# Kernel tuning notes

Measured on AMD Instinct MI355X. Metric: run time of the kernel, lower is better.

The kernel has to match this reference:

```python
import jax, jax.numpy as jnp
import numpy as np
from jax import lax

B, INC1, INC2, H, W = 8, 64, 128, 128, 128
EPS = 1e-5  # BatchNorm eps; inference mode with running_mean=0, running_var=1


def leaky(x):
    return jnp.where(x >= 0, x, 0.01 * x)


def conv2d(x, w, pad=0, dil=1, groups=1):
    return lax.conv_general_dilated(
        x, w, (1, 1), [(pad, pad), (pad, pad)], rhs_dilation=(dil, dil),
        dimension_numbers=('NCHW', 'OIHW', 'NCHW'), feature_group_count=groups)


def bnlrelu(x, g, b):
    s = g / jnp.sqrt(1.0 + EPS)
    return leaky(x * s[None, :, None, None] + b[None, :, None, None])


def interp_bilinear_ac(x, oh, ow):
    # bilinear, align_corners=True (matches F.interpolate)
    ih, iw = x.shape[-2], x.shape[-1]
    ys = jnp.linspace(0.0, ih - 1.0, oh)
    xs = jnp.linspace(0.0, iw - 1.0, ow)
    y0 = jnp.floor(ys).astype(jnp.int32); y1 = jnp.minimum(y0 + 1, ih - 1)
    x0 = jnp.floor(xs).astype(jnp.int32); x1 = jnp.minimum(x0 + 1, iw - 1)
    wy = (ys - y0)[:, None]; wx = xs - x0
    rows = x[..., y0, :] * (1.0 - wy) + x[..., y1, :] * wy
    return rows[..., x0] * (1.0 - wx) + rows[..., x1] * wx


def se_layer(x, w1, w2):
    y = x.mean(axis=(2, 3))                     # [B, C]
    y = jax.nn.sigmoid(leaky(y @ w1.T) @ w2.T)  # squeeze-excite gates
    return x * y[:, :, None, None]


def dyn_multidil(f2, k):
    # per-sample depthwise conv with input-dependent 5x5 kernels, 3 dilations
    C = k.shape[1]
    def per_sample(fi, ki):
        xi = fi[None]            # [1, C, H, W]
        wi = ki[:, None, :, :]   # [C, 1, 5, 5]
        r = conv2d(xi, wi, pad=2, dil=1, groups=C)
        r = r + conv2d(xi, wi, pad=4, dil=2, groups=C)
        r = r + conv2d(xi, wi, pad=6, dil=3, groups=C)
        return r[0]
    out = jax.vmap(per_sample)(f2, k)
    return out.at[0].set(f2[0])  # original python loop starts at i=1: sample 0 untouched


def _forward(x1, k, conv1_w, conv1_g, conv1_b, conv2_w, conv2_g, conv2_b,
             conv_w, conv_bias, c0_w, c0_g, c0_b, attc_w, attc_g, attc_b,
             c05_w, c05_g, c05_b, conv0a_w, conv0a_g, conv0a_b,
             conv0b_w, conv0b_g, conv0b_b, se_w1, se_w2):
    h, w = x1.shape[2], x1.shape[3]
    kse = interp_bilinear_ac(k, h, w)                       # [B, inc1, H, W]
    va = x1.mean(axis=(2, 3), keepdims=True)                # AdaptiveAvgPool2d(1)
    bias = conv_bias[None, :, None, None]
    # MaxPool2d(1) is identity, so conv(vm) == conv(x1); bias added in both terms
    fuseadd = (conv2d(va, conv_w) + bias) + (conv2d(x1, conv_w) + bias)
    fuseadd = fuseadd * kse + fuseadd
    att = jax.nn.sigmoid(fuseadd)
    eadd = bnlrelu(conv2d(fuseadd, c0_w, pad=1), c0_g, c0_b)
    A1 = jax.nn.sigmoid(bnlrelu(conv2d(eadd, attc_w, pad=1), attc_g, attc_b))
    att = se_layer(att, se_w1, se_w2)
    f1 = bnlrelu(conv2d(x1, conv1_w), conv1_g, conv1_b)
    f2 = bnlrelu(conv2d(x1, conv2_w), conv2_g, conv2_b)
    out1 = bnlrelu(conv2d(f1, c0_w, pad=1), c0_g, c0_b)
    out1 = out1 * kse + out1
    A2 = jax.nn.sigmoid(bnlrelu(conv2d(out1, attc_w, pad=1), attc_g, attc_b))
    out2 = dyn_multidil(f2, k)
    out2 = out2 * kse + out2
    out2conv = bnlrelu(conv2d(out2, c05_w, pad=2), c05_g, c05_b)
    fuseout2 = A1 * A2 * out2conv
    finout2 = bnlrelu(conv2d(fuseout2, c05_w, pad=2), c05_g, c05_b)
    eout2 = finout2 + out2conv + f2
    out2 = bnlrelu(conv2d(eout2, c05_w, pad=2), c05_g, c05_b)
    out = jnp.concatenate([out1, out2], axis=1)             # [B, 2*inc1, H, W]
    out = bnlrelu(conv2d(out, conv0a_w), conv0a_g, conv0a_b)
    out = bnlrelu(conv2d(out, conv0b_w, pad=1), conv0b_g, conv0b_b)
    return att * out * A1


def setup_inputs() -> dict:
    key = jax.random.key(0)
    ks = jax.random.split(key, 32)
    f32 = jnp.float32
    def w(i, shape, s=0.05):
        return jax.random.normal(ks[i], shape, f32) * s
    return {
        'x1': jax.random.normal(ks[0], (B, INC2, H, W), f32),
        'k': jax.random.normal(ks[1], (B, INC1, 5, 5), f32) * 0.2,
        'conv1_w': w(2, (INC1, INC2, 1, 1)),
        'conv1_g': 1.0 + w(3, (INC1,)),
        'conv1_b': w(4, (INC1,)),
        'conv2_w': w(5, (INC1, INC2, 1, 1)),
        'conv2_g': 1.0 + w(6, (INC1,)),
        'conv2_b': w(7, (INC1,)),
        'conv_w': w(8, (INC1, INC2, 1, 1)),
        'conv_bias': w(9, (INC1,)),
        'c0_w': w(10, (INC1, INC1, 3, 3)),
        'c0_g': 1.0 + w(11, (INC1,)),
        'c0_b': w(12, (INC1,)),
        'attc_w': w(13, (INC1, INC1, 3, 3)),
        'attc_g': 1.0 + w(14, (INC1,)),
        'attc_b': w(15, (INC1,)),
        'c05_w': w(16, (INC1, INC1, 5, 5)),
        'c05_g': 1.0 + w(17, (INC1,)),
        'c05_b': w(18, (INC1,)),
        'conv0a_w': w(19, (INC1, 2 * INC1, 1, 1)),
        'conv0a_g': 1.0 + w(20, (INC1,)),
        'conv0a_b': w(21, (INC1,)),
        'conv0b_w': w(22, (INC1, INC1, 3, 3)),
        'conv0b_g': 1.0 + w(23, (INC1,)),
        'conv0b_b': w(24, (INC1,)),
        'se_w1': w(25, (INC1 // 16, INC1)),
        'se_w2': w(26, (INC1, INC1 // 16)),
    }


def reference(x1, k, conv1_w, conv1_g, conv1_b, conv2_w, conv2_g, conv2_b,
              conv_w, conv_bias, c0_w, c0_g, c0_b, attc_w, attc_g, attc_b,
              c05_w, c05_g, c05_b, conv0a_w, conv0a_g, conv0a_b,
              conv0b_w, conv0b_g, conv0b_b, se_w1, se_w2):
    return _forward(x1, k, conv1_w, conv1_g, conv1_b, conv2_w, conv2_g, conv2_b,
                    conv_w, conv_bias, c0_w, c0_g, c0_b, attc_w, attc_g, attc_b,
                    c05_w, c05_g, c05_b, conv0a_w, conv0a_g, conv0a_b,
                    conv0b_w, conv0b_g, conv0b_b, se_w1, se_w2)
```

## Files before the change

### kernel.cpp

```cpp
#include <hip/hip_runtime.h>
#include <math.h>

#define HW 16384
#define EPSC 1.00001f

typedef short bf16x8 __attribute__((ext_vector_type(8)));
typedef float f32x4 __attribute__((ext_vector_type(4)));

static __device__ __forceinline__ unsigned short f2bf(float f) {
    unsigned int u = __float_as_uint(f);
    unsigned int r = (u + 0x7fffu + ((u >> 16) & 1u)) >> 16;
    return (unsigned short)r;
}
static __device__ __forceinline__ float bf2f(unsigned short u) {
    return __uint_as_float(((unsigned int)u) << 16);
}

__global__ void mean_hw_kernel(const float* __restrict__ x, float* __restrict__ out) {
    int blk = blockIdx.x;
    const float4* p4 = (const float4*)(x + (size_t)blk * HW);
    float s = 0.f;
    for (int i = threadIdx.x; i < HW / 4; i += 256) {
        float4 v = p4[i];
        s += v.x + v.y + v.z + v.w;
    }
    for (int off = 32; off > 0; off >>= 1) s += __shfl_down(s, off, 64);
    __shared__ float red[4];
    int lane = threadIdx.x & 63, wid = threadIdx.x >> 6;
    if (lane == 0) red[wid] = s;
    __syncthreads();
    if (threadIdx.x == 0)
        out[blk] = (red[0] + red[1] + red[2] + red[3]) * (1.0f / (float)HW);
}

__global__ void convva_kernel(const float* __restrict__ va, const float* __restrict__ cw,
                              float* __restrict__ out) {
    int t = threadIdx.x;
    int b = t >> 6, co = t & 63;
    float s = 0.f;
    for (int ci = 0; ci < 128; ci++) s = fmaf(cw[co * 128 + ci], va[b * 128 + ci], s);
    out[t] = s;
}

__global__ void att_mean_part(const unsigned short* __restrict__ att0, float* __restrict__ part) {
    int s = blockIdx.x, b = blockIdx.y;
    int c = threadIdx.x & 63, pr = threadIdx.x >> 6;
    const unsigned short* p = att0 + ((size_t)b * HW + s * 1024 + pr * 256) * 64 + c;
    float acc = 0.f;
    for (int i = 0; i < 256; i++) acc += bf2f(p[(size_t)i * 64]);
    __shared__ float red[4][64];
    red[pr][c] = acc;
    __syncthreads();
    if (threadIdx.x < 64)
        part[(b * 16 + s) * 64 + threadIdx.x] =
            red[0][threadIdx.x] + red[1][threadIdx.x] + red[2][threadIdx.x] + red[3][threadIdx.x];
}

__global__ void se_mlp_kernel(const float* __restrict__ part, const float* __restrict__ w1,
                              const float* __restrict__ w2, float* __restrict__ scale) {
    __shared__ float t[8][4];
    __shared__ float ym[8][64];
    int tid = threadIdx.x;
    {
        int b = tid >> 6, c = tid & 63;
        float s = 0.f;
        for (int i = 0; i < 16; i++) s += part[(b * 16 + i) * 64 + c];
        ym[b][c] = s * (1.0f / (float)HW);
    }
    __syncthreads();
    if (tid < 32) {
        int b = tid >> 2, h = tid & 3;
        float s = 0.f;
        for (int ci = 0; ci < 64; ci++) s = fmaf(ym[b][ci], w1[h * 64 + ci], s);
        t[b][h] = s >= 0.f ? s : 0.01f * s;
    }
    __syncthreads();
    int b = tid >> 6, c = tid & 63;
    float s = 0.f;
    for (int h = 0; h < 4; h++) s = fmaf(t[b][h], w2[c * 4 + h], s);
    scale[b * 64 + c] = 1.0f / (1.0f + __expf(-s));
}

__device__ __forceinline__ float kse_val(const float* kt, int y, int x) {
    float ys = y * (4.0f / 127.0f);
    int y0 = (int)ys; if (y0 > 4) y0 = 4;
    int y1 = min(y0 + 1, 4);
    float wy = ys - (float)y0;
    float xs = x * (4.0f / 127.0f);
    int x0 = (int)xs; if (x0 > 4) x0 = 4;
    int x1 = min(x0 + 1, 4);
    float wx = xs - (float)x0;
    float r0 = kt[y0 * 5 + x0] * (1.f - wx) + kt[y0 * 5 + x1] * wx;
    float r1 = kt[y1 * 5 + x0] * (1.f - wx) + kt[y1 * 5 + x1] * wx;
    return r0 * (1.f - wy) + r1 * wy;
}

__global__ void repack_x1_kernel(const float* __restrict__ x1,
                                 unsigned short* __restrict__ xa,
                                 unsigned short* __restrict__ xb) {
    __shared__ float t[64][65];
    int b = blockIdx.y;
    int p0 = blockIdx.x * 64;
    for (int h = 0; h < 2; ++h) {
        const float* src = x1 + ((size_t)b * 128 + h * 64) * HW + p0;
        __syncthreads();
        for (int e = threadIdx.x; e < 4096; e += 256) {
            int ci = e >> 6, px = e & 63;
            t[ci][px] = src[(size_t)ci * HW + px];
        }
        __syncthreads();
        unsigned short* dst = (h == 0 ? xa : xb) + ((size_t)b * HW + p0) * 64;
        for (int e = threadIdx.x; e < 4096; e += 256) {
            int px = e >> 6, ci = e & 63;
            dst[(size_t)px * 64 + ci] = f2bf(t[ci][px]);
        }
    }
}

__global__ void prep_w_kernel(const float* __restrict__ src, unsigned short* __restrict__ dst,
                              int CO, int CI, int K, int co_total, int co_off) {
    int idx = blockIdx.x * 256 + threadIdx.x;
    int total = CO * CI * K * K;
    if (idx >= total) return;
    int kx = idx % K, t1 = idx / K;
    int ky = t1 % K, t2 = t1 / K;
    int ci = t2 % CI, co = t2 / CI;
    int tap = ky * K + kx, chunk = ci >> 5, k32 = ci & 31;
    int kc = tap * (CI >> 5) + chunk;
    dst[((size_t)kc * co_total + co_off + co) * 32 + k32] = f2bf(src[idx]);
}

template<int KSZ, int CI>
__global__ __launch_bounds__(256, 3) void conv_mfma(
    const unsigned short* __restrict__ Xa, const unsigned short* __restrict__ Xb,
    const unsigned short* __restrict__ Wp,
    const float* __restrict__ g, const float* __restrict__ bb,
    const float* __restrict__ kk,
    const unsigned short* __restrict__ eB, const unsigned short* __restrict__ eC,
    float* __restrict__ out_f32, unsigned short* __restrict__ out_bf,
    unsigned short* __restrict__ aux_bf, int emode)
{
    constexpr int TH  = 8;
    constexpr int PAD = KSZ / 2;
    constexpr int TWX = 16 + 2 * PAD;
    constexpr int TWY = TH + 2 * PAD;
    constexpr int CHUNKS = CI / 32;
    constexpr int NT = 2;
    constexpr int CI8 = CI / 8;
    constexpr int CI8SH = (CI == 64) ? 3 : 4;
    constexpr int NTAP = KSZ * KSZ;
    constexpr int WSLAB = 64 * 32 * CHUNKS;
    constexpr int NBUF = (KSZ == 1) ? 1 : 2;
    constexpr int NSTG = WSLAB / (8 * 256);
    __shared__ unsigned short xs[TWY * TWX * CI];
    __shared__ unsigned short ws[NBUF * WSLAB];

    const int b = blockIdx.y;
    const int ty = (blockIdx.x >> 3) * TH, tx = (blockIdx.x & 7) * 16;
    const int tid = threadIdx.x;
    const int lane = tid & 63, wv = tid >> 6;
    const int n = lane & 15, quad = lane >> 4;

    uint4 wst[NSTG];
    {
        const uint4* gw = (const uint4*)Wp;
#pragma unroll
        for (int s = 0; s < NSTG; ++s) wst[s] = gw[tid + s * 256];
    }
    for (int e = tid; e < TWY * TWX * CI8; e += 256) {
        int ci8 = e & (CI8 - 1);
        int pxl = e >> CI8SH;
        int xx = pxl % TWX, yy = pxl / TWX;
        int gy = ty + yy - PAD, gx = tx + xx - PAD;
        uint4 v = {0u, 0u, 0u, 0u};
        if (gy >= 0 && gy < 128 && gx >= 0 && gx < 128) {
            const unsigned short* src = Xa;
            int c8 = ci8;
            if (CI == 128 && ci8 >= 8) { src = Xb; c8 = ci8 - 8; }
            v = *(const uint4*)(src + (((size_t)b * HW + gy * 128 + gx) * 64 + c8 * 8));
        }
        *(uint4*)(&xs[(size_t)pxl * CI + ((ci8 ^ (pxl & 7)) << 3)]) = v;
    }
    {
        uint4* lw = (uint4*)ws;
#pragma unroll
        for (int s = 0; s < NSTG; ++s) lw[tid + s * 256] = wst[s];
    }
    __syncthreads();

    f32x4 acc[4][NT];
#pragma unroll
    for (int mb = 0; mb < 4; ++mb)
#pragma unroll
        for (int nt = 0; nt < NT; ++nt) acc[mb][nt] = (f32x4){0.f, 0.f, 0.f, 0.f};

    const int r0 = wv * NT;
    for (int tap = 0; tap < NTAP; ++tap) {
        if (KSZ > 1 && tap + 1 < NTAP) {
            const uint4* gw = (const uint4*)Wp + (size_t)(tap + 1) * (WSLAB / 8);
#pragma unroll
            for (int s = 0; s < NSTG; ++s) wst[s] = gw[tid + s * 256];
        }
        const unsigned short* wl = ws + ((NBUF == 2) ? (tap & 1) * WSLAB : 0);
        const int ky = tap / KSZ, kx = tap - ky * KSZ;
#pragma unroll
        for (int ch = 0; ch < CHUNKS; ++ch) {
            bf16x8 af[4];
#pragma unroll
            for (int mb = 0; mb < 4; ++mb)
                af[mb] = *(const bf16x8*)(wl + (ch * 64 + mb * 16 + n) * 32 + quad * 8);
            bf16x8 bfr[NT];
#pragma unroll
            for (int nt = 0; nt < NT; ++nt) {
                int pxl = (r0 + nt + ky) * TWX + n + kx;
                bfr[nt] = *(const bf16x8*)(&xs[(size_t)pxl * CI +
                                               (((ch * 4 + quad) ^ (pxl & 7)) << 3)]);
            }
#pragma unroll
            for (int mb = 0; mb < 4; ++mb)
#pragma unroll
                for (int nt = 0; nt < NT; ++nt)
                    acc[mb][nt] = __builtin_amdgcn_mfma_f32_16x16x32_bf16(
                        af[mb], bfr[nt], acc[mb][nt], 0, 0, 0);
        }
        if (KSZ > 1 && tap + 1 < NTAP) {
            uint4* lw = (uint4*)(ws + ((tap + 1) & 1) * WSLAB);
#pragma unroll
            for (int s = 0; s < NSTG; ++s) lw[tid + s * 256] = wst[s];
            __syncthreads();
        }
    }

    const float rs = rsqrtf(EPSC);
#pragma unroll
    for (int mb = 0; mb < 4; ++mb) {
#pragma unroll
        for (int nt = 0; nt < NT; ++nt) {
            const int py = ty + r0 + nt;
            const int px = tx + n;
            const size_t pix = (size_t)b * HW + py * 128 + px;
            const int co0 = mb * 16 + quad * 4;
            float v4[4];
#pragma unroll
            for (int rg = 0; rg < 4; ++rg) {
                int co = co0 + rg;
                float v = acc[mb][nt][rg];
                v = fmaf(v, g[co] * rs, bb[co]);
                v = v >= 0.f ? v : 0.01f * v;
                if (emode == 1 || emode == 6) v = 1.0f / (1.0f + __expf(-v));
                else if (emode == 2)
                    v *= (1.0f + kse_val(kk + (size_t)(b * 64 + co) * 25, py, px));
                v4[rg] = v;
            }
            if (emode == 6) {
                ushort4 e = *(const ushort4*)(eB + pix * 64 + co0);
                *(ushort4*)(out_bf + pix * 64 + co0) = (ushort4){
                    f2bf(v4[0] * bf2f(e.x)), f2bf(v4[1] * bf2f(e.y)),
                    f2bf(v4[2] * bf2f(e.z)), f2bf(v4[3] * bf2f(e.w))};
            } else if (emode == 4) {
                *(ushort4*)(out_bf + pix * 64 + co0) =
                    (ushort4){f2bf(v4[0]), f2bf(v4[1]), f2bf(v4[2]), f2bf(v4[3])};
                ushort4 e = *(const ushort4*)(eB + pix * 64 + co0);
                *(ushort4*)(aux_bf + pix * 64 + co0) = (ushort4){
                    f2bf(v4[0] * bf2f(e.x)), f2bf(v4[1] * bf2f(e.y)),
                    f2bf(v4[2] * bf2f(e.z)), f2bf(v4[3] * bf2f(e.w))};
            } else if (emode == 5) {
                ushort4 e1 = *(const ushort4*)(eB + pix * 64 + co0);
                ushort4 e2 = *(const ushort4*)(eC + pix * 64 + co0);
                *(ushort4*)(out_bf + pix * 64 + co0) = (ushort4){
                    f2bf(v4[0] + bf2f(e1.x) + bf2f(e2.x)), f2bf(v4[1] + bf2f(e1.y) + bf2f(e2.y)),
                    f2bf(v4[2] + bf2f(e1.z) + bf2f(e2.z)), f2bf(v4[3] + bf2f(e1.w) + bf2f(e2.w))};
            } else {
                if (out_bf)
                    *(ushort4*)(out_bf + pix * 64 + co0) =
                        (ushort4){f2bf(v4[0]), f2bf(v4[1]), f2bf(v4[2]), f2bf(v4[3])};
                if (out_f32) {
#pragma unroll
                    for (int rg = 0; rg < 4; ++rg)
                        out_f32[(size_t)(b * 64 + co0 + rg) * HW + py * 128 + px] = v4[rg];
                }
            }
        }
    }
}

__global__ __launch_bounds__(256, 2) void conv1x1_triple(
    const unsigned short* __restrict__ Xa, const unsigned short* __restrict__ Xb,
    const unsigned short* __restrict__ Wp,
    const float* __restrict__ cva, const float* __restrict__ cbias,
    const float* __restrict__ g1, const float* __restrict__ b1,
    const float* __restrict__ g2, const float* __restrict__ b2,
    const float* __restrict__ kk,
    unsigned short* __restrict__ fuse_bf, unsigned short* __restrict__ att0_bf,
    unsigned short* __restrict__ f1_bf,
    float* __restrict__ f2_f32, unsigned short* __restrict__ f2_bf)
{
    constexpr int CI = 128;
    __shared__ unsigned short xs[128 * CI];
    __shared__ unsigned short ws[4 * 192 * 32];
    const int b = blockIdx.y;
    const int ty = (blockIdx.x >> 3) * 8, tx = (blockIdx.x & 7) * 16;
    const int tid = threadIdx.x;
    const int lane = tid & 63, wv = tid >> 6;
    const int n = lane & 15, quad = lane >> 4;

    {
        const uint4* gw = (const uint4*)Wp;
        uint4* lw = (uint4*)ws;
#pragma unroll
        for (int s = 0; s < 12; ++s) lw[tid + s * 256] = gw[tid + s * 256];
    }
    for (int e = tid; e < 128 * 16; e += 256) {
        int ci8 = e & 15, pxl = e >> 4;
        int gy = ty + (pxl >> 4), gx = tx + (pxl & 15);
        const unsigned short* src = (ci8 >= 8) ? Xb : Xa;
        int c8 = ci8 & 7;
        uint4 v = *(const uint4*)(src + (((size_t)b * HW + gy * 128 + gx) * 64 + c8 * 8));
        *(uint4*)(&xs[(size_t)pxl * CI + ((ci8 ^ (pxl & 7)) << 3)]) = v;
    }
    __syncthreads();

    f32x4 acc[12][2];
#pragma unroll
    for (int mb = 0; mb < 12; ++mb)
#pragma unroll
        for (int nt = 0; nt < 2; ++nt) acc[mb][nt] = (f32x4){0.f, 0.f, 0.f, 0.f};

    const int r0 = wv * 2;
#pragma unroll
    for (int ch = 0; ch < 4; ++ch) {
        bf16x8 bfr[2];
#pragma unroll
        for (int nt = 0; nt < 2; ++nt) {
            int pxl = (r0 + nt) * 16 + n;
            bfr[nt] = *(const bf16x8*)(&xs[(size_t)pxl * CI +
                                           (((ch * 4 + quad) ^ (pxl & 7)) << 3)]);
        }
#pragma unroll
        for (int mb = 0; mb < 12; ++mb) {
            bf16x8 af = *(const bf16x8*)(ws + (ch * 192 + mb * 16 + n) * 32 + quad * 8);
#pragma unroll
            for (int nt = 0; nt < 2; ++nt)
                acc[mb][nt] = __builtin_amdgcn_mfma_f32_16x16x32_bf16(
                    af, bfr[nt], acc[mb][nt], 0, 0, 0);
        }
    }

    const float rs = rsqrtf(EPSC);
#pragma unroll
    for (int mb = 0; mb < 12; ++mb) {
#pragma unroll
        for (int nt = 0; nt < 2; ++nt) {
            const int py = ty + r0 + nt;
            const int px = tx + n;
            const size_t pix = (size_t)b * HW + py * 128 + px;
            const int cg = mb * 16 + quad * 4;
            if (mb < 4) {
                float v4[4], s4[4];
#pragma unroll
                for (int rg = 0; rg < 4; ++rg) {
                    int co = cg + rg;
                    float base = cva[b * 64 + co] + 2.0f * cbias[co];
                    float fa = (acc[mb][nt][rg] + base) *
                               (1.0f + kse_val(kk + (size_t)(b * 64 + co) * 25, py, px));
                    v4[rg] = fa;
                    s4[rg] = 1.0f / (1.0f + __expf(-fa));
                }
                *(ushort4*)(fuse_bf + pix * 64 + cg) =
                    (ushort4){f2bf(v4[0]), f2bf(v4[1]), f2bf(v4[2]), f2bf(v4[3])};
                *(ushort4*)(att0_bf + pix * 64 + cg) =
                    (ushort4){f2bf(s4[0]), f2bf(s4[1]), f2bf(s4[2]), f2bf(s4[3])};
            } else if (mb < 8) {
                int co0 = cg - 64;
                float v4[4];
#pragma unroll
                for (int rg = 0; rg < 4; ++rg) {
                    float v = fmaf(acc[mb][nt][rg], g1[co0 + rg] * rs, b1[co0 + rg]);
                    v4[rg] = v >= 0.f ? v : 0.01f * v;
                }
                *(ushort4*)(f1_bf + pix * 64 + co0) =
                    (ushort4){f2bf(v4[0]), f2bf(v4[1]), f2bf(v4[2]), f2bf(v4[3])};
            } else {
                int co0 = cg - 128;
                float v4[4];
#pragma unroll
                for (int rg = 0; rg < 4; ++rg) {
                    float v = fmaf(acc[mb][nt][rg], g2[co0 + rg] * rs, b2[co0 + rg]);
                    v4[rg] = v >= 0.f ? v : 0.01f * v;
                    f2_f32[(size_t)(b * 64 + co0 + rg) * HW + py * 128 + px] = v4[rg];
                }
                *(ushort4*)(f2_bf + pix * 64 + co0) =
                    (ushort4){f2bf(v4[0]), f2bf(v4[1]), f2bf(v4[2]), f2bf(v4[3])};
            }
        }
    }
}

__global__ __launch_bounds__(256) void dyndil_kernel(const float* __restrict__ f2,
                                                     const float* __restrict__ kk,
                                                     unsigned short* __restrict__ out2bf) {
    __shared__ float xl[44][148];
    int b = blockIdx.x >> 8, c = (blockIdx.x >> 2) & 63, band = blockIdx.x & 3;
    int y0 = band * 32;
    int tid = threadIdx.x;
    int r = tid >> 3, s = tid & 7;
    int x0 = s * 16;
    int y = y0 + r;
    const float* xp = f2 + (size_t)(b * 64 + c) * HW;
    const float* kt = kk + (size_t)(b * 64 + c) * 25;
    float acc[16];

    if (b != 0) {
        for (int e = tid; e < 44 * 148; e += 256) {
            int rr = e / 148, cc = e - rr * 148;
            int yy = y0 + rr - 6, xx = cc - 8;
            float v = 0.f;
            if (yy >= 0 && yy < 128 && xx >= 0 && xx < 128)
                v = xp[yy * 128 + xx];
            xl[rr][cc] = v;
        }
        float kw[25];
#pragma unroll
        for (int i = 0; i < 25; i++) kw[i] = kt[i];
        __syncthreads();
#pragma unroll
        for (int e = 0; e < 16; e++) acc[e] = 0.f;
        int rr = r + 6;
        float win[32];
#define LOADROW(OFF) { const float4* p4 = (const float4*)&xl[rr + (OFF)][x0]; \
        float4 t0=p4[0],t1=p4[1],t2=p4[2],t3=p4[3],t4=p4[4],t5=p4[5],t6=p4[6],t7=p4[7]; \
        win[0]=t0.x;win[1]=t0.y;win[2]=t0.z;win[3]=t0.w; win[4]=t1.x;win[5]=t1.y;win[6]=t1.z;win[7]=t1.w; \
        win[8]=t2.x;win[9]=t2.y;win[10]=t2.z;win[11]=t2.w; win[12]=t3.x;win[13]=t3.y;win[14]=t3.z;win[15]=t3.w; \
        win[16]=t4.x;win[17]=t4.y;win[18]=t4.z;win[19]=t4.w; win[20]=t5.x;win[21]=t5.y;win[22]=t5.z;win[23]=t5.w; \
        win[24]=t6.x;win[25]=t6.y;win[26]=t6.z;win[27]=t6.w; win[28]=t7.x;win[29]=t7.y;win[30]=t7.z;win[31]=t7.w; }
#define APPLY(DIL, I) { \
        _Pragma("unroll") for (int j = 0; j < 5; j++) { \
            float wv = kw[(I)*5 + j]; int o = 8 + (j - 2) * (DIL); \
            _Pragma("unroll") for (int e2 = 0; e2 < 16; e2++) \
                acc[e2] = fmaf(wv, win[e2 + o], acc[e2]); } }
        LOADROW(-6) APPLY(3,0)
        LOADROW(-4) APPLY(2,0)
        LOADROW(-3) APPLY(3,1)
        LOADROW(-2) APPLY(1,0) APPLY(2,1)
        LOADROW(-1) APPLY(1,1)
        LOADROW(0)  APPLY(1,2) APPLY(2,2) APPLY(3,2)
        LOADROW(1)  APPLY(1,3)
        LOADROW(2)  APPLY(1,4) APPLY(2,3)
        LOADROW(3)  APPLY(3,3)
        LOADROW(4)  APPLY(2,4)
        LOADROW(6)  APPLY(3,4)
#undef LOADROW
#undef APPLY
    } else {
        const float4* p4 = (const float4*)(xp + y * 128 + x0);
#pragma unroll
        for (int i = 0; i < 4; i++) {
            float4 v = p4[i];
            acc[i*4] = v.x; acc[i*4+1] = v.y; acc[i*4+2] = v.z; acc[i*4+3] = v.w;
        }
    }
    float ys = y * (4.0f / 127.0f);
    int yi0 = (int)ys; if (yi0 > 4) yi0 = 4;
    int yi1 = yi0 + 1; if (yi1 > 4) yi1 = 4;
    float wy = ys - (float)yi0;
    float ry0 = kt[yi0*5+0] * (1.f-wy) + kt[yi1*5+0] * wy;
    float ry1 = kt[yi0*5+1] * (1.f-wy) + kt[yi1*5+1] * wy;
    float ry2 = kt[yi0*5+2] * (1.f-wy) + kt[yi1*5+2] * wy;
    float ry3 = kt[yi0*5+3] * (1.f-wy) + kt[yi1*5+3] * wy;
    float ry4 = kt[yi0*5+4] * (1.f-wy) + kt[yi1*5+4] * wy;
    unsigned short* op = out2bf + ((size_t)b * HW + (size_t)y * 128 + x0) * 64 + c;
#pragma unroll
    for (int e = 0; e < 16; e++) {
        int x = x0 + e;
        float xs2 = x * (4.0f / 127.0f);
        int xi0 = (int)xs2; if (xi0 > 4) xi0 = 4;
        float wx = xs2 - (float)xi0;
        float a = xi0==0 ? ry0 : xi0==1 ? ry1 : xi0==2 ? ry2 : xi0==3 ? ry3 : ry4;
        float bs = xi0>=3 ? ry4 : (xi0==2 ? ry3 : (xi0==1 ? ry2 : ry1));
        float kv = a + (bs - a) * wx;
        op[(size_t)e * 64] = f2bf(acc[e] * (1.0f + kv));
    }
}

__global__ void final_kernel(const unsigned short* __restrict__ att0,
                             const float* __restrict__ scale,
                             const unsigned short* __restrict__ outb,
                             const unsigned short* __restrict__ a1,
                             float* __restrict__ o) {
    __shared__ float t[64][65];
    int b = blockIdx.y;
    int p0 = blockIdx.x * 64;
    int tid = threadIdx.x;
    for (int e = tid; e < 4096; e += 256) {
        int px = e >> 6, c = e & 63;
        size_t idx = ((size_t)b * HW + p0 + px) * 64 + c;
        t[c][px] = bf2f(att0[idx]) * scale[b * 64 + c] * bf2f(outb[idx]) * bf2f(a1[idx]);
    }
    __syncthreads();
    for (int e = tid; e < 4096; e += 256) {
        int c = e >> 6, px = e & 63;
        o[((size_t)b * 64 + c) * HW + p0 + px] = t[c][px];
    }
}

extern "C" void kernel_launch(void* const* d_in, const int* in_sizes, int n_in,
                              void* d_out, int out_size, void* d_ws, size_t ws_size,
                              hipStream_t stream) {
    const float* x1      = (const float*)d_in[0];
    const float* kk      = (const float*)d_in[1];
    const float* conv1_w = (const float*)d_in[2];
    const float* conv1_g = (const float*)d_in[3];
    const float* conv1_b = (const float*)d_in[4];
    const float* conv2_w = (const float*)d_in[5];
    const float* conv2_g = (const float*)d_in[6];
    const float* conv2_b = (const float*)d_in[7];
    const float* conv_w  = (const float*)d_in[8];
    const float* conv_bias = (const float*)d_in[9];
    const float* c0_w  = (const float*)d_in[10];
    const float* c0_g  = (const float*)d_in[11];
    const float* c0_b  = (const float*)d_in[12];
    const float* attc_w = (const float*)d_in[13];
    const float* attc_g = (const float*)d_in[14];
    const float* attc_b = (const float*)d_in[15];
    const float* c05_w = (const float*)d_in[16];
    const float* c05_g = (const float*)d_in[17];
    const float* c05_b = (const float*)d_in[18];
    const float* conv0a_w = (const float*)d_in[19];
    const float* conv0a_g = (const float*)d_in[20];
    const float* conv0a_b = (const float*)d_in[21];
    const float* conv0b_w = (const float*)d_in[22];
    const float* conv0b_g = (const float*)d_in[23];
    const float* conv0b_b = (const float*)d_in[24];
    const float* se_w1 = (const float*)d_in[25];
    const float* se_w2 = (const float*)d_in[26];

    const size_t U = (size_t)8 * HW * 64 * 2;
    unsigned char* P = (unsigned char*)d_ws;
    unsigned short* x1a        = (unsigned short*)(P + 0 * U);
    unsigned short* x1b        = (unsigned short*)(P + 1 * U);
    unsigned short* att0_bf    = (unsigned short*)(P + 2 * U);
    unsigned short* fuse_bf    = (unsigned short*)(P + 3 * U);
    unsigned short* f1_bf      = (unsigned short*)(P + 4 * U);
    float*          f2         = (float*)         (P + 5 * U);
    unsigned short* f2_bf      = (unsigned short*)(P + 7 * U);
    unsigned short* A1_bf      = (unsigned short*)(P + 8 * U);
    unsigned short* eadd_bf    = (unsigned short*)(P + 9 * U);
    unsigned short* out1_bf    = (unsigned short*)(P + 10 * U);
    unsigned short* A12_bf     = (unsigned short*)(P + 11 * U);
    unsigned short* out2_bf     = x1a;
    unsigned short* oc_bf       = x1b;
    unsigned short* fuseout2_bf = fuse_bf;
    unsigned short* eout2_bf    = f1_bf;
    unsigned short* out2fin_bf  = eadd_bf;
    unsigned short* outb_bf     = out1_bf;
    unsigned short* outa_bf     = A12_bf;

    unsigned char* W0 = P + 12 * U;
    unsigned short* Wp1   = (unsigned short*)(W0);
    unsigned short* Wc0   = (unsigned short*)(W0 + 49152);
    unsigned short* Wattc = (unsigned short*)(W0 + 122880);
    unsigned short* Wc05  = (unsigned short*)(W0 + 196608);
    unsigned short* Wc0a  = (unsigned short*)(W0 + 401408);
    unsigned short* Wc0b  = (unsigned short*)(W0 + 417792);
    float* va   = (float*)(W0 + 491520);
    float* cva  = va + 1024;
    float* part = cva + 512;
    float* sesc = part + 8192;

    const dim3 gconv(128, 8);

    mean_hw_kernel<<<1024, 256, 0, stream>>>(x1, va);
    convva_kernel<<<1, 512, 0, stream>>>(va, conv_w, cva);
    repack_x1_kernel<<<dim3(256, 8), 256, 0, stream>>>(x1, x1a, x1b);
    prep_w_kernel<<<32, 256, 0, stream>>>(conv_w,   Wp1, 64, 128, 1, 192, 0);
    prep_w_kernel<<<32, 256, 0, stream>>>(conv1_w,  Wp1, 64, 128, 1, 192, 64);
    prep_w_kernel<<<32, 256, 0, stream>>>(conv2_w,  Wp1, 64, 128, 1, 192, 128);
    prep_w_kernel<<<144, 256, 0, stream>>>(c0_w,    Wc0,   64, 64, 3, 64, 0);
    prep_w_kernel<<<144, 256, 0, stream>>>(attc_w,  Wattc, 64, 64, 3, 64, 0);
    prep_w_kernel<<<400, 256, 0, stream>>>(c05_w,   Wc05,  64, 64, 5, 64, 0);
    prep_w_kernel<<<32, 256, 0, stream>>>(conv0a_w, Wc0a,  64, 128, 1, 64, 0);
    prep_w_kernel<<<144, 256, 0, stream>>>(conv0b_w, Wc0b, 64, 64, 3, 64, 0);

    conv1x1_triple<<<gconv, 256, 0, stream>>>(x1a, x1b, Wp1, cva, conv_bias,
        conv1_g, conv1_b, conv2_g, conv2_b, kk, fuse_bf, att0_bf, f1_bf, f2, f2_bf);

    att_mean_part<<<dim3(16, 8), 256, 0, stream>>>(att0_bf, part);
    se_mlp_kernel<<<1, 512, 0, stream>>>(part, se_w1, se_w2, sesc);

    dyndil_kernel<<<2048, 256, 0, stream>>>(f2, kk, out2_bf);

    conv_mfma<3, 64><<<gconv, 256, 0, stream>>>(fuse_bf, nullptr, Wc0,
        c0_g, c0_b, kk, nullptr, nullptr, nullptr, eadd_bf, nullptr, 0);
    conv_mfma<3, 64><<<gconv, 256, 0, stream>>>(eadd_bf, nullptr, Wattc,
        attc_g, attc_b, kk, nullptr, nullptr, nullptr, A1_bf, nullptr, 1);
    conv_mfma<3, 64><<<gconv, 256, 0, stream>>>(f1_bf, nullptr, Wc0,
        c0_g, c0_b, kk, nullptr, nullptr, nullptr, out1_bf, nullptr, 2);
    conv_mfma<3, 64><<<gconv, 256, 0, stream>>>(out1_bf, nullptr, Wattc,
        attc_g, attc_b, kk, A1_bf, nullptr, nullptr, A12_bf, nullptr, 6);

    conv_mfma<5, 64><<<gconv, 256, 0, stream>>>(out2_bf, nullptr, Wc05,
        c05_g, c05_b, kk, A12_bf, nullptr, nullptr, oc_bf, fuseout2_bf, 4);
    conv_mfma<5, 64><<<gconv, 256, 0, stream>>>(fuseout2_bf, nullptr, Wc05,
        c05_g, c05_b, kk, oc_bf, f2_bf, nullptr, eout2_bf, nullptr, 5);
    conv_mfma<5, 64><<<gconv, 256, 0, stream>>>(eout2_bf, nullptr, Wc05,
        c05_g, c05_b, kk, nullptr, nullptr, nullptr, out2fin_bf, nullptr, 0);

    conv_mfma<1, 128><<<gconv, 256, 0, stream>>>(out1_bf, out2fin_bf, Wc0a,
        conv0a_g, conv0a_b, kk, nullptr, nullptr, nullptr, outa_bf, nullptr, 0);
    conv_mfma<3, 64><<<gconv, 256, 0, stream>>>(outa_bf, nullptr, Wc0b,
        conv0b_g, conv0b_b, kk, nullptr, nullptr, nullptr, outb_bf, nullptr, 0);
    final_kernel<<<dim3(256, 8), 256, 0, stream>>>(att0_bf, sesc, outb_bf, A1_bf, (float*)d_out);
}
```

Before: 633.7 us.

## Switch spatial convs to 32x32x16 MFMA with 16x16 tiles and lane-packed weights

The 3x3 and 5x5 convolutions move from 16x16x32 MFMA on 8x16 pixel tiles to 32x32x16 MFMA on 16x16 tiles. Each wave now computes 64 pixels by 64 output channels. Weights are repacked per lane so A fragments load with contiguous, conflict-free LDS reads, and the halo overhead per output pixel drops. The 1x1 conv gets its own specialised kernel with preloaded lane-packed weights. The cost is more accumulator registers, occupancy lowered to 2 blocks per SM, and half as many blocks (512) spread over the GPU.

```diff
diff --git a/kernel.cpp b/kernel.cpp
--- a/kernel.cpp
+++ b/kernel.cpp
@@ -6,6 +6,7 @@
 
 typedef short bf16x8 __attribute__((ext_vector_type(8)));
 typedef float f32x4 __attribute__((ext_vector_type(4)));
+typedef float f32x16 __attribute__((ext_vector_type(16)));
 
 static __device__ __forceinline__ unsigned short f2bf(float f) {
     unsigned int u = __float_as_uint(f);
@@ -130,104 +131,227 @@
     dst[((size_t)kc * co_total + co_off + co) * 32 + k32] = f2bf(src[idx]);
 }
 
-template<int KSZ, int CI>
-__global__ __launch_bounds__(256, 3) void conv_mfma(
-    const unsigned short* __restrict__ Xa, const unsigned short* __restrict__ Xb,
+__global__ void prep_w32_kernel(const float* __restrict__ src, unsigned short* __restrict__ dst,
+                                int CO, int CI, int K) {
+    int idx = blockIdx.x * 256 + threadIdx.x;
+    int total = CO * CI * K * K;
+    if (idx >= total) return;
+    int kx = idx % K, t1 = idx / K;
+    int ky = t1 % K, t2 = t1 / K;
+    int ci = t2 % CI, co = t2 / CI;
+    int tap = ky * K + kx;
+    int kstep = ci >> 4, khalf = (ci >> 3) & 1, j = ci & 7;
+    int l = khalf * 32 + (co & 31), mb = co >> 5;
+    dst[(((size_t)(tap * 4 + kstep) * 2 + mb) * 64 + l) * 8 + j] = f2bf(src[idx]);
+}
+
+__global__ void prep_w16_kernel(const float* __restrict__ src, unsigned short* __restrict__ dst,
+                                int CO, int CI) {
+    int idx = blockIdx.x * 256 + threadIdx.x;
+    if (idx >= CO * CI) return;
+    int ci = idx % CI, co = idx / CI;
+    int ch = ci >> 5, q = (ci >> 3) & 3, j = ci & 7;
+    int l = q * 16 + (co & 15), mb = co >> 4;
+    dst[(((size_t)ch * 4 + mb) * 64 + l) * 8 + j] = f2bf(src[idx]);
+}
+
+template<int KSZ>
+__global__ __launch_bounds__(256, 2) void conv_mfma32(
+    const unsigned short* __restrict__ Xa,
     const unsigned short* __restrict__ Wp,
     const float* __restrict__ g, const float* __restrict__ bb,
     const float* __restrict__ kk,
     const unsigned short* __restrict__ eB, const unsigned short* __restrict__ eC,
-    float* __restrict__ out_f32, unsigned short* __restrict__ out_bf,
-    unsigned short* __restrict__ aux_bf, int emode)
+    unsigned short* __restrict__ out_bf, unsigned short* __restrict__ aux_bf, int emode)
 {
-    constexpr int TH  = 8;
     constexpr int PAD = KSZ / 2;
     constexpr int TWX = 16 + 2 * PAD;
-    constexpr int TWY = TH + 2 * PAD;
-    constexpr int CHUNKS = CI / 32;
-    constexpr int NT = 2;
-    constexpr int CI8 = CI / 8;
-    constexpr int CI8SH = (CI == 64) ? 3 : 4;
+    constexpr int TWY = 16 + 2 * PAD;
     constexpr int NTAP = KSZ * KSZ;
-    constexpr int WSLAB = 64 * 32 * CHUNKS;
-    constexpr int NBUF = (KSZ == 1) ? 1 : 2;
-    constexpr int NSTG = WSLAB / (8 * 256);
-    __shared__ unsigned short xs[TWY * TWX * CI];
-    __shared__ unsigned short ws[NBUF * WSLAB];
+    constexpr int WSLAB = 4 * 2 * 64 * 8;
+    __shared__ unsigned short xs[TWY * TWX * 64];
+    __shared__ unsigned short ws[2 * WSLAB];
 
     const int b = blockIdx.y;
-    const int ty = (blockIdx.x >> 3) * TH, tx = (blockIdx.x & 7) * 16;
+    const int ty = (blockIdx.x >> 3) * 16, tx = (blockIdx.x & 7) * 16;
+    const int tid = threadIdx.x;
+    const int lane = tid & 63, wv = tid >> 6;
+    const int n32 = lane & 31, khalf = lane >> 5;
+
+    int rr[2], cc2[2];
+#pragma unroll
+    for (int nt = 0; nt < 2; ++nt) {
+        int p = wv * 64 + nt * 32 + n32;
+        rr[nt] = p >> 4; cc2[nt] = p & 15;
+    }
+
+    uint4 wst[2];
+    {
+        const uint4* gw = (const uint4*)Wp;
+#pragma unroll
+        for (int s = 0; s < 2; ++s) wst[s] = gw[tid + s * 256];
+    }
+    for (int e = tid; e < TWY * TWX * 8; e += 256) {
+        int ci8 = e & 7, pxl = e >> 3;
+        int xx = pxl % TWX, yy = pxl / TWX;
+        int gy = ty + yy - PAD, gx = tx + xx - PAD;
+        uint4 v = {0u, 0u, 0u, 0u};
+        if (gy >= 0 && gy < 128 && gx >= 0 && gx < 128)
+            v = *(const uint4*)(Xa + (((size_t)b * HW + gy * 128 + gx) * 64 + ci8 * 8));
+        *(uint4*)(&xs[(size_t)pxl * 64 + ((ci8 ^ (pxl & 7)) << 3)]) = v;
+    }
+    {
+        uint4* lw = (uint4*)ws;
+#pragma unroll
+        for (int s = 0; s < 2; ++s) lw[tid + s * 256] = wst[s];
+    }
+    __syncthreads();
+
+    f32x16 acc[2][2];
+#pragma unroll
+    for (int mb = 0; mb < 2; ++mb)
+#pragma unroll
+        for (int nt = 0; nt < 2; ++nt)
+#pragma unroll
+            for (int i = 0; i < 16; ++i) acc[mb][nt][i] = 0.f;
+
+    for (int tap = 0; tap < NTAP; ++tap) {
+        if (tap + 1 < NTAP) {
+            const uint4* gw = (const uint4*)Wp + (size_t)(tap + 1) * (WSLAB / 8);
+#pragma unroll
+            for (int s = 0; s < 2; ++s) wst[s] = gw[tid + s * 256];
+        }
+        const unsigned short* wl = ws + (tap & 1) * WSLAB;
+        const int ky = tap / KSZ, kx = tap - ky * KSZ;
+        int pxl0 = (rr[0] + ky) * TWX + cc2[0] + kx;
+        int pxl1 = (rr[1] + ky) * TWX + cc2[1] + kx;
+        int sw0 = (pxl0 & 7), sw1 = (pxl1 & 7);
+#pragma unroll
+        for (int kstep = 0; kstep < 4; ++kstep) {
+            bf16x8 af0 = *(const bf16x8*)(wl + ((kstep * 2 + 0) * 64 + lane) * 8);
+            bf16x8 af1 = *(const bf16x8*)(wl + ((kstep * 2 + 1) * 64 + lane) * 8);
+            int gidx = kstep * 2 + khalf;
+            bf16x8 b0 = *(const bf16x8*)(&xs[(size_t)pxl0 * 64 + ((gidx ^ sw0) << 3)]);
+            bf16x8 b1 = *(const bf16x8*)(&xs[(size_t)pxl1 * 64 + ((gidx ^ sw1) << 3)]);
+            acc[0][0] = __builtin_amdgcn_mfma_f32_32x32x16_bf16(af0, b0, acc[0][0], 0, 0, 0);
+            acc[0][1] = __builtin_amdgcn_mfma_f32_32x32x16_bf16(af0, b1, acc[0][1], 0, 0, 0);
+            acc[1][0] = __builtin_amdgcn_mfma_f32_32x32x16_bf16(af1, b0, acc[1][0], 0, 0, 0);
+            acc[1][1] = __builtin_amdgcn_mfma_f32_32x32x16_bf16(af1, b1, acc[1][1], 0, 0, 0);
+        }
+        if (tap + 1 < NTAP) {
+            uint4* lw = (uint4*)(ws + ((tap + 1) & 1) * WSLAB);
+#pragma unroll
+            for (int s = 0; s < 2; ++s) lw[tid + s * 256] = wst[s];
+            __syncthreads();
+        }
+    }
+
+    const float rs = rsqrtf(EPSC);
+#pragma unroll
+    for (int mb = 0; mb < 2; ++mb) {
+#pragma unroll
+        for (int nt = 0; nt < 2; ++nt) {
+            const int py = ty + rr[nt];
+            const int px = tx + cc2[nt];
+            const size_t pix = (size_t)b * HW + py * 128 + px;
+#pragma unroll
+            for (int rq = 0; rq < 4; ++rq) {
+                const int co0 = mb * 32 + rq * 8 + khalf * 4;
+                float v4[4];
+#pragma unroll
+                for (int rg = 0; rg < 4; ++rg) {
+                    int co = co0 + rg;
+                    float v = acc[mb][nt][rq * 4 + rg];
+                    v = fmaf(v, g[co] * rs, bb[co]);
+                    v = v >= 0.f ? v : 0.01f * v;
+                    if (emode == 1 || emode == 6) v = 1.0f / (1.0f + __expf(-v));
+                    else if (emode == 2)
+                        v *= (1.0f + kse_val(kk + (size_t)(b * 64 + co) * 25, py, px));
+                    v4[rg] = v;
+                }
+                if (emode == 6) {
+                    ushort4 e = *(const ushort4*)(eB + pix * 64 + co0);
+                    *(ushort4*)(out_bf + pix * 64 + co0) = (ushort4){
+                        f2bf(v4[0] * bf2f(e.x)), f2bf(v4[1] * bf2f(e.y)),
+                        f2bf(v4[2] * bf2f(e.z)), f2bf(v4[3] * bf2f(e.w))};
+                } else if (emode == 4) {
+                    *(ushort4*)(out_bf + pix * 64 + co0) =
+                        (ushort4){f2bf(v4[0]), f2bf(v4[1]), f2bf(v4[2]), f2bf(v4[3])};
+                    ushort4 e = *(const ushort4*)(eB + pix * 64 + co0);
+                    *(ushort4*)(aux_bf + pix * 64 + co0) = (ushort4){
+                        f2bf(v4[0] * bf2f(e.x)), f2bf(v4[1] * bf2f(e.y)),
+                        f2bf(v4[2] * bf2f(e.z)), f2bf(v4[3] * bf2f(e.w))};
+                } else if (emode == 5) {
+                    ushort4 e1 = *(const ushort4*)(eB + pix * 64 + co0);
+                    ushort4 e2 = *(const ushort4*)(eC + pix * 64 + co0);
+                    *(ushort4*)(out_bf + pix * 64 + co0) = (ushort4){
+                        f2bf(v4[0] + bf2f(e1.x) + bf2f(e2.x)),
+                        f2bf(v4[1] + bf2f(e1.y) + bf2f(e2.y)),
+                        f2bf(v4[2] + bf2f(e1.z) + bf2f(e2.z)),
+                        f2bf(v4[3] + bf2f(e1.w) + bf2f(e2.w))};
+                } else {
+                    *(ushort4*)(out_bf + pix * 64 + co0) =
+                        (ushort4){f2bf(v4[0]), f2bf(v4[1]), f2bf(v4[2]), f2bf(v4[3])};
+                }
+            }
+        }
+    }
+}
+
+__global__ __launch_bounds__(256, 2) void conv_mfma1x1(
+    const unsigned short* __restrict__ Xa, const unsigned short* __restrict__ Xb,
+    const unsigned short* __restrict__ Wp,
+    const float* __restrict__ g, const float* __restrict__ bb,
+    unsigned short* __restrict__ out_bf)
+{
+    constexpr int CI = 128;
+    __shared__ unsigned short xs[128 * CI];
+    __shared__ unsigned short ws[4 * 4 * 64 * 8];
+    const int b = blockIdx.y;
+    const int ty = (blockIdx.x >> 3) * 8, tx = (blockIdx.x & 7) * 16;
     const int tid = threadIdx.x;
     const int lane = tid & 63, wv = tid >> 6;
     const int n = lane & 15, quad = lane >> 4;
 
-    uint4 wst[NSTG];
     {
         const uint4* gw = (const uint4*)Wp;
-#pragma unroll
-        for (int s = 0; s < NSTG; ++s) wst[s] = gw[tid + s * 256];
-    }
-    for (int e = tid; e < TWY * TWX * CI8; e += 256) {
-        int ci8 = e & (CI8 - 1);
-        int pxl = e >> CI8SH;
-        int xx = pxl % TWX, yy = pxl / TWX;
-        int gy = ty + yy - PAD, gx = tx + xx - PAD;
-        uint4 v = {0u, 0u, 0u, 0u};
-        if (gy >= 0 && gy < 128 && gx >= 0 && gx < 128) {
-            const unsigned short* src = Xa;
-            int c8 = ci8;
-            if (CI == 128 && ci8 >= 8) { src = Xb; c8 = ci8 - 8; }
-            v = *(const uint4*)(src + (((size_t)b * HW + gy * 128 + gx) * 64 + c8 * 8));
-        }
+        uint4* lw = (uint4*)ws;
+#pragma unroll
+        for (int s = 0; s < 4; ++s) lw[tid + s * 256] = gw[tid + s * 256];
+    }
+    for (int e = tid; e < 128 * 16; e += 256) {
+        int ci8 = e & 15, pxl = e >> 4;
+        int gy = ty + (pxl >> 4), gx = tx + (pxl & 15);
+        const unsigned short* src = (ci8 >= 8) ? Xb : Xa;
+        int c8 = ci8 & 7;
+        uint4 v = *(const uint4*)(src + (((size_t)b * HW + gy * 128 + gx) * 64 + c8 * 8));
         *(uint4*)(&xs[(size_t)pxl * CI + ((ci8 ^ (pxl & 7)) << 3)]) = v;
     }
-    {
-        uint4* lw = (uint4*)ws;
-#pragma unroll
-        for (int s = 0; s < NSTG; ++s) lw[tid + s * 256] = wst[s];
-    }
     __syncthreads();
 
-    f32x4 acc[4][NT];
+    f32x4 acc[4][2];
 #pragma unroll
     for (int mb = 0; mb < 4; ++mb)
 #pragma unroll
-        for (int nt = 0; nt < NT; ++nt) acc[mb][nt] = (f32x4){0.f, 0.f, 0.f, 0.f};
-
-    const int r0 = wv * NT;
-    for (int tap = 0; tap < NTAP; ++tap) {
-        if (KSZ > 1 && tap + 1 < NTAP) {
-            const uint4* gw = (const uint4*)Wp + (size_t)(tap + 1) * (WSLAB / 8);
-#pragma unroll
-            for (int s = 0; s < NSTG; ++s) wst[s] = gw[tid + s * 256];
-        }
-        const unsigned short* wl = ws + ((NBUF == 2) ? (tap & 1) * WSLAB : 0);
-        const int ky = tap / KSZ, kx = tap - ky * KSZ;
-#pragma unroll
-        for (int ch = 0; ch < CHUNKS; ++ch) {
-            bf16x8 af[4];
-#pragma unroll
-            for (int mb = 0; mb < 4; ++mb)
-                af[mb] = *(const bf16x8*)(wl + (ch * 64 + mb * 16 + n) * 32 + quad * 8);
-            bf16x8 bfr[NT];
-#pragma unroll
-            for (int nt = 0; nt < NT; ++nt) {
-                int pxl = (r0 + nt + ky) * TWX + n + kx;
-                bfr[nt] = *(const bf16x8*)(&xs[(size_t)pxl * CI +
-                                               (((ch * 4 + quad) ^ (pxl & 7)) << 3)]);
-            }
-#pragma unroll
-            for (int mb = 0; mb < 4; ++mb)
-#pragma unroll
-                for (int nt = 0; nt < NT; ++nt)
-                    acc[mb][nt] = __builtin_amdgcn_mfma_f32_16x16x32_bf16(
-                        af[mb], bfr[nt], acc[mb][nt], 0, 0, 0);
-        }
-        if (KSZ > 1 && tap + 1 < NTAP) {
-            uint4* lw = (uint4*)(ws + ((tap + 1) & 1) * WSLAB);
-#pragma unroll
-            for (int s = 0; s < NSTG; ++s) lw[tid + s * 256] = wst[s];
-            __syncthreads();
+        for (int nt = 0; nt < 2; ++nt) acc[mb][nt] = (f32x4){0.f, 0.f, 0.f, 0.f};
+
+    const int r0 = wv * 2;
+#pragma unroll
+    for (int ch = 0; ch < 4; ++ch) {
+        bf16x8 bfr[2];
+#pragma unroll
+        for (int nt = 0; nt < 2; ++nt) {
+            int pxl = (r0 + nt) * 16 + n;
+            bfr[nt] = *(const bf16x8*)(&xs[(size_t)pxl * CI +
+                                           (((ch * 4 + quad) ^ (pxl & 7)) << 3)]);
+        }
+#pragma unroll
+        for (int mb = 0; mb < 4; ++mb) {
+            bf16x8 af = *(const bf16x8*)(ws + ((ch * 4 + mb) * 64 + lane) * 8);
+#pragma unroll
+            for (int nt = 0; nt < 2; ++nt)
+                acc[mb][nt] = __builtin_amdgcn_mfma_f32_16x16x32_bf16(
+                    af, bfr[nt], acc[mb][nt], 0, 0, 0);
         }
     }
 
@@ -235,51 +359,18 @@
 #pragma unroll
     for (int mb = 0; mb < 4; ++mb) {
 #pragma unroll
-        for (int nt = 0; nt < NT; ++nt) {
-            const int py = ty + r0 + nt;
-            const int px = tx + n;
+        for (int nt = 0; nt < 2; ++nt) {
+            const int py = ty + r0 + nt, px = tx + n;
             const size_t pix = (size_t)b * HW + py * 128 + px;
             const int co0 = mb * 16 + quad * 4;
             float v4[4];
 #pragma unroll
             for (int rg = 0; rg < 4; ++rg) {
-                int co = co0 + rg;
-                float v = acc[mb][nt][rg];
-                v = fmaf(v, g[co] * rs, bb[co]);
-                v = v >= 0.f ? v : 0.01f * v;
-                if (emode == 1 || emode == 6) v = 1.0f / (1.0f + __expf(-v));
-                else if (emode == 2)
-                    v *= (1.0f + kse_val(kk + (size_t)(b * 64 + co) * 25, py, px));
-                v4[rg] = v;
+                float v = fmaf(acc[mb][nt][rg], g[co0 + rg] * rs, bb[co0 + rg]);
+                v4[rg] = v >= 0.f ? v : 0.01f * v;
             }
-            if (emode == 6) {
-                ushort4 e = *(const ushort4*)(eB + pix * 64 + co0);
-                *(ushort4*)(out_bf + pix * 64 + co0) = (ushort4){
-                    f2bf(v4[0] * bf2f(e.x)), f2bf(v4[1] * bf2f(e.y)),
-                    f2bf(v4[2] * bf2f(e.z)), f2bf(v4[3] * bf2f(e.w))};
-            } else if (emode == 4) {
-                *(ushort4*)(out_bf + pix * 64 + co0) =
-                    (ushort4){f2bf(v4[0]), f2bf(v4[1]), f2bf(v4[2]), f2bf(v4[3])};
-                ushort4 e = *(const ushort4*)(eB + pix * 64 + co0);
-                *(ushort4*)(aux_bf + pix * 64 + co0) = (ushort4){
-                    f2bf(v4[0] * bf2f(e.x)), f2bf(v4[1] * bf2f(e.y)),
-                    f2bf(v4[2] * bf2f(e.z)), f2bf(v4[3] * bf2f(e.w))};
-            } else if (emode == 5) {
-                ushort4 e1 = *(const ushort4*)(eB + pix * 64 + co0);
-                ushort4 e2 = *(const ushort4*)(eC + pix * 64 + co0);
-                *(ushort4*)(out_bf + pix * 64 + co0) = (ushort4){
-                    f2bf(v4[0] + bf2f(e1.x) + bf2f(e2.x)), f2bf(v4[1] + bf2f(e1.y) + bf2f(e2.y)),
-                    f2bf(v4[2] + bf2f(e1.z) + bf2f(e2.z)), f2bf(v4[3] + bf2f(e1.w) + bf2f(e2.w))};
-            } else {
-                if (out_bf)
-                    *(ushort4*)(out_bf + pix * 64 + co0) =
-                        (ushort4){f2bf(v4[0]), f2bf(v4[1]), f2bf(v4[2]), f2bf(v4[3])};
-                if (out_f32) {
-#pragma unroll
-                    for (int rg = 0; rg < 4; ++rg)
-                        out_f32[(size_t)(b * 64 + co0 + rg) * HW + py * 128 + px] = v4[rg];
-                }
-            }
+            *(ushort4*)(out_bf + pix * 64 + co0) =
+                (ushort4){f2bf(v4[0]), f2bf(v4[1]), f2bf(v4[2]), f2bf(v4[3])};
         }
     }
 }
@@ -567,7 +658,8 @@
     float* part = cva + 512;
     float* sesc = part + 8192;
 
-    const dim3 gconv(128, 8);
+    const dim3 g32(64, 8);
+    const dim3 g16(128, 8);
 
     mean_hw_kernel<<<1024, 256, 0, stream>>>(x1, va);
     convva_kernel<<<1, 512, 0, stream>>>(va, conv_w, cva);
@@ -575,13 +667,13 @@
     prep_w_kernel<<<32, 256, 0, stream>>>(conv_w,   Wp1, 64, 128, 1, 192, 0);
     prep_w_kernel<<<32, 256, 0, stream>>>(conv1_w,  Wp1, 64, 128, 1, 192, 64);
     prep_w_kernel<<<32, 256, 0, stream>>>(conv2_w,  Wp1, 64, 128, 1, 192, 128);
-    prep_w_kernel<<<144, 256, 0, stream>>>(c0_w,    Wc0,   64, 64, 3, 64, 0);
-    prep_w_kernel<<<144, 256, 0, stream>>>(attc_w,  Wattc, 64, 64, 3, 64, 0);
-    prep_w_kernel<<<400, 256, 0, stream>>>(c05_w,   Wc05,  64, 64, 5, 64, 0);
-    prep_w_kernel<<<32, 256, 0, stream>>>(conv0a_w, Wc0a,  64, 128, 1, 64, 0);
-    prep_w_kernel<<<144, 256, 0, stream>>>(conv0b_w, Wc0b, 64, 64, 3, 64, 0);
-
-    conv1x1_triple<<<gconv, 256, 0, stream>>>(x1a, x1b, Wp1, cva, conv_bias,
+    prep_w32_kernel<<<144, 256, 0, stream>>>(c0_w,    Wc0,   64, 64, 3);
+    prep_w32_kernel<<<144, 256, 0, stream>>>(attc_w,  Wattc, 64, 64, 3);
+    prep_w32_kernel<<<400, 256, 0, stream>>>(c05_w,   Wc05,  64, 64, 5);
+    prep_w16_kernel<<<32, 256, 0, stream>>>(conv0a_w, Wc0a,  64, 128);
+    prep_w32_kernel<<<144, 256, 0, stream>>>(conv0b_w, Wc0b, 64, 64, 3);
+
+    conv1x1_triple<<<g16, 256, 0, stream>>>(x1a, x1b, Wp1, cva, conv_bias,
         conv1_g, conv1_b, conv2_g, conv2_b, kk, fuse_bf, att0_bf, f1_bf, f2, f2_bf);
 
     att_mean_part<<<dim3(16, 8), 256, 0, stream>>>(att0_bf, part);
@@ -589,25 +681,25 @@
 
     dyndil_kernel<<<2048, 256, 0, stream>>>(f2, kk, out2_bf);
 
-    conv_mfma<3, 64><<<gconv, 256, 0, stream>>>(fuse_bf, nullptr, Wc0,
-        c0_g, c0_b, kk, nullptr, nullptr, nullptr, eadd_bf, nullptr, 0);
-    conv_mfma<3, 64><<<gconv, 256, 0, stream>>>(eadd_bf, nullptr, Wattc,
-        attc_g, attc_b, kk, nullptr, nullptr, nullptr, A1_bf, nullptr, 1);
-    conv_mfma<3, 64><<<gconv, 256, 0, stream>>>(f1_bf, nullptr, Wc0,
-        c0_g, c0_b, kk, nullptr, nullptr, nullptr, out1_bf, nullptr, 2);
-    conv_mfma<3, 64><<<gconv, 256, 0, stream>>>(out1_bf, nullptr, Wattc,
-        attc_g, attc_b, kk, A1_bf, nullptr, nullptr, A12_bf, nullptr, 6);
-
-    conv_mfma<5, 64><<<gconv, 256, 0, stream>>>(out2_bf, nullptr, Wc05,
-        c05_g, c05_b, kk, A12_bf, nullptr, nullptr, oc_bf, fuseout2_bf, 4);
-    conv_mfma<5, 64><<<gconv, 256, 0, stream>>>(fuseout2_bf, nullptr, Wc05,
-        c05_g, c05_b, kk, oc_bf, f2_bf, nullptr, eout2_bf, nullptr, 5);
-    conv_mfma<5, 64><<<gconv, 256, 0, stream>>>(eout2_bf, nullptr, Wc05,
-        c05_g, c05_b, kk, nullptr, nullptr, nullptr, out2fin_bf, nullptr, 0);
-
-    conv_mfma<1, 128><<<gconv, 256, 0, stream>>>(out1_bf, out2fin_bf, Wc0a,
-        conv0a_g, conv0a_b, kk, nullptr, nullptr, nullptr, outa_bf, nullptr, 0);
-    conv_mfma<3, 64><<<gconv, 256, 0, stream>>>(outa_bf, nullptr, Wc0b,
-        conv0b_g, conv0b_b, kk, nullptr, nullptr, nullptr, outb_bf, nullptr, 0);
+    conv_mfma32<3><<<g32, 256, 0, stream>>>(fuse_bf, Wc0,
+        c0_g, c0_b, kk, nullptr, nullptr, eadd_bf, nullptr, 0);
+    conv_mfma32<3><<<g32, 256, 0, stream>>>(eadd_bf, Wattc,
+        attc_g, attc_b, kk, nullptr, nullptr, A1_bf, nullptr, 1);
+    conv_mfma32<3><<<g32, 256, 0, stream>>>(f1_bf, Wc0,
+        c0_g, c0_b, kk, nullptr, nullptr, out1_bf, nullptr, 2);
+    conv_mfma32<3><<<g32, 256, 0, stream>>>(out1_bf, Wattc,
+        attc_g, attc_b, kk, A1_bf, nullptr, A12_bf, nullptr, 6);
+
+    conv_mfma32<5><<<g32, 256, 0, stream>>>(out2_bf, Wc05,
+        c05_g, c05_b, kk, A12_bf, nullptr, oc_bf, fuseout2_bf, 4);
+    conv_mfma32<5><<<g32, 256, 0, stream>>>(fuseout2_bf, Wc05,
+        c05_g, c05_b, kk, oc_bf, f2_bf, eout2_bf, nullptr, 5);
+    conv_mfma32<5><<<g32, 256, 0, stream>>>(eout2_bf, Wc05,
+        c05_g, c05_b, kk, nullptr, nullptr, out2fin_bf, nullptr, 0);
+
+    conv_mfma1x1<<<g16, 256, 0, stream>>>(out1_bf, out2fin_bf, Wc0a,
+        conv0a_g, conv0a_b, outa_bf);
+    conv_mfma32<3><<<g32, 256, 0, stream>>>(outa_bf, Wc0b,
+        conv0b_g, conv0b_b, kk, nullptr, nullptr, outb_bf, nullptr, 0);
     final_kernel<<<dim3(256, 8), 256, 0, stream>>>(att0_bf, sesc, outb_bf, A1_bf, (float*)d_out);
 }
```

Result: slower. 677.7 us (+6.9%).
